# Performance work log

Hardware: AMD Instinct MI355X
Metric: run time of the kernel (lower is better)

The kernel has to match this reference:

```python
import jax, jax.numpy as jnp
import numpy as np

N = 1_000_000  # total_voxels
V = 128        # volume_size


def setup_inputs() -> dict:
    key = jax.random.key(0)
    ks = jax.random.split(key, 10)
    inds = jax.random.randint(ks[0], (N, 3), 0, V, dtype=jnp.int32)
    reference_values = jax.random.normal(ks[1], (1, N), dtype=jnp.float32)
    # SIREN-ish init scales: ~1/sqrt(fan_in) keeps sin() inputs O(1); tiny final
    # layer scale keeps delta_coords sub-voxel (as training would).
    W0 = jax.random.normal(ks[2], (3 * N, 8), dtype=jnp.float32) / np.float32(np.sqrt(3 * N))
    W1 = jax.random.normal(ks[3], (8, 8), dtype=jnp.float32) / np.float32(np.sqrt(8))
    W2 = jax.random.normal(ks[4], (8, 8), dtype=jnp.float32) / np.float32(np.sqrt(8))
    W3 = jax.random.normal(ks[5], (8, 8), dtype=jnp.float32) / np.float32(np.sqrt(8))
    W4 = jax.random.normal(ks[6], (8, 8), dtype=jnp.float32) / np.float32(np.sqrt(8))
    W5 = jax.random.normal(ks[7], (8, 4 * N), dtype=jnp.float32) * np.float32(0.01 / np.sqrt(8))
    z8 = jnp.zeros((8,), jnp.float32)
    return {
        "inds": inds, "reference_values": reference_values,
        "W0": W0, "b0": z8, "W1": W1, "b1": z8, "W2": W2, "b2": z8,
        "W3": W3, "b3": z8, "W4": W4, "b4": z8,
        "W5": W5, "b5": jnp.zeros((4 * N,), jnp.float32),
        "volume_size": V,
    }


def reference(inds, reference_values, W0, b0, W1, b1, W2, b2, W3, b3, W4, b4,
              W5, b5, volume_size):
    n = inds.shape[0]
    factor = 0.5 * volume_size
    # normalized coords buffer: stack (z,y,x) columns -> (1, N, 3) in [-1, 1)
    coords_n = (jnp.stack([inds[:, 2], inds[:, 1], inds[:, 0]], axis=1)[None]
                .astype(jnp.float32) - factor) / factor
    # tiny SIREN MLP on the flattened coord vector (1, 3N)
    x = jnp.sin(coords_n.reshape(1, -1) @ W0 + b0)
    for W, b in ((W1, b1), (W2, b2), (W3, b3), (W4, b4)):
        x = x + jnp.sin(x @ W + b)
    x = (x @ W5 + b5).reshape(1, n, 4)          # (1, N, 4)
    delta_coords, delta_values = x[..., :3], x[..., 3]
    values = jax.nn.relu(reference_values + delta_values)      # (1, N)
    coords = factor * (coords_n + delta_coords) + factor       # voxel-space, (1, N, 3)
    # trilinear 8-corner splat
    bposf = jnp.floor(coords)
    bposi = bposf.astype(jnp.int32)                             # (1, N, 3)
    f = coords - bposf
    fx, fy, fz = f[..., 0], f[..., 1], f[..., 2]
    gx, gy, gz = 1.0 - fx, 1.0 - fy, 1.0 - fz
    bamp = jnp.concatenate([
        values * gx * gy * gz, values * fx * gy * gz,
        values * gx * fy * gz, values * gx * gy * fz,
        values * gx * fy * fz, values * fx * gy * fz,
        values * fx * fy * gz, values * fx * fy * fz,
    ], axis=1)                                                  # (1, 8N)
    offs = jnp.array([[0, 0, 0], [1, 0, 0], [0, 1, 0], [0, 0, 1],
                      [0, 1, 1], [1, 0, 1], [1, 1, 0], [1, 1, 1]], jnp.int32)
    bpos = jnp.concatenate([bposi + o for o in offs], axis=1)   # (1, 8N, 3)
    vol0 = jnp.zeros((values.shape[0], volume_size, volume_size, volume_size),
                     jnp.float32)

    def scatter(vol, p, a):  # out-of-bounds corners are dropped (jax default)
        return vol.at[p[:, 2], p[:, 1], p[:, 0]].add(a)

    return jax.vmap(scatter, in_axes=(0, 0, 0))(vol0, bpos, bamp)
```

## Files before the change

kernel.cpp:

```cpp
#include <hip/hip_runtime.h>
#include <hip/hip_bf16.h>

constexpr int V = 128;
constexpr int NTILES = 512;
constexpr int TD = 17;
constexpr int TSIZE = TD * TD * TD;
constexpr int TPAD = 5120;
constexpr int NS = 16;
constexpr int CAPS = 256;
constexpr int CNT_INTS = NS * NTILES * 16;

__global__ __launch_bounds__(256) void k_reduce_w0(
    const int* __restrict__ inds, const float* __restrict__ W0,
    float* __restrict__ partials, float4* __restrict__ vol4,
    int4* __restrict__ cnt4, int threeN) {
  int g = blockIdx.x * 256 + threadIdx.x;
  vol4[g] = make_float4(0.f, 0.f, 0.f, 0.f);
  if (cnt4 && g < CNT_INTS / 4) cnt4[g] = make_int4(0, 0, 0, 0);

  float acc[8];
#pragma unroll
  for (int k = 0; k < 8; ++k) acc[k] = 0.f;

  int stride = gridDim.x * blockDim.x;
  for (int j = g; j < threeN; j += stride) {
    int c = j % 3;
    float cval = ((float)inds[j + 2 - 2 * c] - 64.0f) * 0.015625f;
    const float4* w = (const float4*)(W0 + (size_t)j * 8);
    float4 a = w[0];
    float4 b = w[1];
    acc[0] += cval * a.x; acc[1] += cval * a.y;
    acc[2] += cval * a.z; acc[3] += cval * a.w;
    acc[4] += cval * b.x; acc[5] += cval * b.y;
    acc[6] += cval * b.z; acc[7] += cval * b.w;
  }

#pragma unroll
  for (int off = 32; off > 0; off >>= 1) {
#pragma unroll
    for (int k = 0; k < 8; ++k) acc[k] += __shfl_down(acc[k], off);
  }

  __shared__ float red[4][8];
  int wave = threadIdx.x >> 6;
  int lane = threadIdx.x & 63;
  if (lane == 0) {
#pragma unroll
    for (int k = 0; k < 8; ++k) red[wave][k] = acc[k];
  }
  __syncthreads();
  if (threadIdx.x < 8) {
    int k = threadIdx.x;
    partials[(size_t)blockIdx.x * 8 + k] = red[0][k] + red[1][k] + red[2][k] + red[3][k];
  }
}

__global__ __launch_bounds__(256) void k_mlp(
    const float* __restrict__ partials, int nb,
    const float* __restrict__ b0,
    const float* __restrict__ W1, const float* __restrict__ b1,
    const float* __restrict__ W2, const float* __restrict__ b2,
    const float* __restrict__ W3, const float* __restrict__ b3,
    const float* __restrict__ W4, const float* __restrict__ b4,
    float* __restrict__ x8_out) {
  __shared__ float red[256];
  __shared__ float accv[8];
  int tid = threadIdx.x;
  int k = tid & 7;
  float s = 0.f;
  for (int b = tid >> 3; b < nb; b += 32) s += partials[(size_t)b * 8 + k];
  red[tid] = s;
  __syncthreads();
  if (tid < 8) {
    float t = 0.f;
    for (int j = tid; j < 256; j += 8) t += red[j];
    accv[tid] = t;
  }
  __syncthreads();
  if (tid == 0) {
    float x[8];
#pragma unroll
    for (int kk = 0; kk < 8; ++kk) x[kk] = sinf(accv[kk] + b0[kk]);
    const float* Ws[4] = {W1, W2, W3, W4};
    const float* bs[4] = {b1, b2, b3, b4};
    for (int l = 0; l < 4; ++l) {
      float t[8];
#pragma unroll
      for (int kk = 0; kk < 8; ++kk) {
        float ss = bs[l][kk];
#pragma unroll
        for (int j = 0; j < 8; ++j) ss += x[j] * Ws[l][j * 8 + kk];
        t[kk] = ss;
      }
#pragma unroll
      for (int kk = 0; kk < 8; ++kk) x[kk] += sinf(t[kk]);
    }
#pragma unroll
    for (int kk = 0; kk < 8; ++kk) x8_out[kk] = x[kk];
  }
}

__device__ inline int tile_of(float cx, float cy, float cz) {
  int bx = (int)floorf(cx), by = (int)floorf(cy), bz = (int)floorf(cz);
  int tx = min(max(bx, 0), V - 1) >> 4;
  int ty = min(max(by, 0), V - 1) >> 4;
  int tz = min(max(bz, 0), V - 1) >> 4;
  return (tz << 6) | (ty << 3) | tx;
}

__device__ inline void scatter_direct(float* vol, float cx, float cy, float cz,
                                      float value) {
  float bxf = floorf(cx), byf = floorf(cy), bzf = floorf(cz);
  int bx = (int)bxf, by = (int)byf, bz = (int)bzf;
  float fx = cx - bxf, fy = cy - byf, fz = cz - bzf;
  float gx = 1.f - fx, gy = 1.f - fy, gz = 1.f - fz;
#pragma unroll
  for (int dz = 0; dz < 2; ++dz)
#pragma unroll
    for (int dy = 0; dy < 2; ++dy)
#pragma unroll
      for (int dx = 0; dx < 2; ++dx) {
        float w = value * (dx ? fx : gx) * (dy ? fy : gy) * (dz ? fz : gz);
        int px = bx + dx, py = by + dy, pz = bz + dz;
        if (px < 0) px += V;
        if (py < 0) py += V;
        if (pz < 0) pz += V;
        if ((unsigned)px < (unsigned)V && (unsigned)py < (unsigned)V &&
            (unsigned)pz < (unsigned)V)
          atomicAdd(vol + ((size_t)pz * V * V + (size_t)py * V + px), w);
      }
}

__global__ __launch_bounds__(256) void k_decode_scatter(
    const int* __restrict__ inds, const float* __restrict__ refv,
    const float* __restrict__ W5, const float* __restrict__ b5,
    const float* __restrict__ x8_buf, float4* __restrict__ srt,
    int* __restrict__ cnt, float* __restrict__ vol, int N) {
  __shared__ float x8[8];
  if (threadIdx.x < 8) x8[threadIdx.x] = x8_buf[threadIdx.x];
  __syncthreads();

  int i = blockIdx.x * 256 + threadIdx.x;
  if (i >= N) return;

  const size_t fourN = (size_t)4 * N;
  float4 o = *(const float4*)(b5 + (size_t)4 * i);
  float out0 = o.x, out1 = o.y, out2 = o.z, out3 = o.w;
#pragma unroll
  for (int k = 0; k < 8; ++k) {
    float xv = x8[k];
    float4 w = *(const float4*)(W5 + (size_t)k * fourN + (size_t)4 * i);
    out0 += xv * w.x; out1 += xv * w.y; out2 += xv * w.z; out3 += xv * w.w;
  }
  float value = refv[i] + out3;
  value = value > 0.f ? value : 0.f;
  if (value <= 0.f) return;

  int i0 = inds[3 * i], i1 = inds[3 * i + 1], i2 = inds[3 * i + 2];
  float cx = (((float)i2 - 64.0f) * 0.015625f + out0) * 64.0f + 64.0f;
  float cy = (((float)i1 - 64.0f) * 0.015625f + out1) * 64.0f + 64.0f;
  float cz = (((float)i0 - 64.0f) * 0.015625f + out2) * 64.0f + 64.0f;

  int t = tile_of(cx, cy, cz);
  int s = blockIdx.x & (NS - 1);
  int slot = s * NTILES + t;
  int pos = atomicAdd(&cnt[slot * 16], 1);
  if (pos < CAPS) {
    srt[(size_t)slot * CAPS + pos] = make_float4(cx, cy, cz, value);
  } else {
    scatter_direct(vol, cx, cy, cz, value);
  }
}

__global__ __launch_bounds__(256) void k_tile(
    const float4* __restrict__ srt, const int* __restrict__ cnt,
    float* __restrict__ priv, float* __restrict__ vol) {
  __shared__ float tl[TSIZE];
  int t = blockIdx.x;
  int ox = (t & 7) << 4, oy = ((t >> 3) & 7) << 4, oz = (t >> 6) << 4;
  for (int j = threadIdx.x; j < TSIZE; j += 256) tl[j] = 0.f;
  __syncthreads();

  for (int s = 0; s < NS; ++s) {
    int slot = s * NTILES + t;
    int c = min(cnt[slot * 16], CAPS);
    const float4* base = srt + (size_t)slot * CAPS;
    for (int i = threadIdx.x; i < c; i += 256) {
      float4 r = base[i];
      float bxf = floorf(r.x), byf = floorf(r.y), bzf = floorf(r.z);
      int bx = (int)bxf, by = (int)byf, bz = (int)bzf;
      float fx = r.x - bxf, fy = r.y - byf, fz = r.z - bzf;
      float gx = 1.f - fx, gy = 1.f - fy, gz = 1.f - fz;
      float value = r.w;

#pragma unroll
      for (int dz = 0; dz < 2; ++dz) {
#pragma unroll
        for (int dy = 0; dy < 2; ++dy) {
#pragma unroll
          for (int dx = 0; dx < 2; ++dx) {
            float w = value * (dx ? fx : gx) * (dy ? fy : gy) * (dz ? fz : gz);
            int px = bx + dx, py = by + dy, pz = bz + dz;
            if (px < 0) px += V;
            if (py < 0) py += V;
            if (pz < 0) pz += V;
            if (px >= V || py >= V || pz >= V) continue;
            int lx = px - ox, ly = py - oy, lz = pz - oz;
            if ((unsigned)lx < (unsigned)TD && (unsigned)ly < (unsigned)TD &&
                (unsigned)lz < (unsigned)TD) {
              atomicAdd(&tl[lz * (TD * TD) + ly * TD + lx], w);
            } else {
              atomicAdd(vol + ((size_t)pz * V * V + (size_t)py * V + px), w);
            }
          }
        }
      }
    }
  }
  __syncthreads();
  for (int j = threadIdx.x; j < TSIZE; j += 256) priv[(size_t)t * TPAD + j] = tl[j];
}

__global__ __launch_bounds__(256) void k_gather(const float* __restrict__ priv,
                                                float* __restrict__ vol) {
  int idx = blockIdx.x * 256 + threadIdx.x;
  int x = idx & 127, y = (idx >> 7) & 127, z = idx >> 14;
  float s = vol[idx];
  int txs[2] = {x >> 4, (x >> 4) - 1}, lxs[2] = {x & 15, 16};
  int tys[2] = {y >> 4, (y >> 4) - 1}, lys[2] = {y & 15, 16};
  int tzs[2] = {z >> 4, (z >> 4) - 1}, lzs[2] = {z & 15, 16};
  int nx = ((x & 15) == 0 && x > 0) ? 2 : 1;
  int ny = ((y & 15) == 0 && y > 0) ? 2 : 1;
  int nz = ((z & 15) == 0 && z > 0) ? 2 : 1;
  for (int iz = 0; iz < nz; ++iz)
    for (int iy = 0; iy < ny; ++iy)
      for (int ix = 0; ix < nx; ++ix) {
        int t = (tzs[iz] << 6) | (tys[iy] << 3) | txs[ix];
        s += priv[(size_t)t * TPAD + lzs[iz] * (TD * TD) + lys[iy] * TD + lxs[ix]];
      }
  vol[idx] = s;
}

__global__ __launch_bounds__(256) void k_scatter(
    const int* __restrict__ inds, const float* __restrict__ refv,
    const float* __restrict__ W5, const float* __restrict__ b5,
    const float* __restrict__ x8_buf, float* __restrict__ vol, int N) {
  __shared__ float x8[8];
  if (threadIdx.x < 8) x8[threadIdx.x] = x8_buf[threadIdx.x];
  __syncthreads();
  int i = blockIdx.x * blockDim.x + threadIdx.x;
  if (i >= N) return;
  const size_t fourN = (size_t)4 * N;
  float4 o = *(const float4*)(b5 + (size_t)4 * i);
  float out0 = o.x, out1 = o.y, out2 = o.z, out3 = o.w;
#pragma unroll
  for (int k = 0; k < 8; ++k) {
    float xv = x8[k];
    float4 w = *(const float4*)(W5 + (size_t)k * fourN + (size_t)4 * i);
    out0 += xv * w.x; out1 += xv * w.y; out2 += xv * w.z; out3 += xv * w.w;
  }
  float value = refv[i] + out3;
  value = value > 0.f ? value : 0.f;
  int i0 = inds[3 * i], i1 = inds[3 * i + 1], i2 = inds[3 * i + 2];
  float cx = (((float)i2 - 64.0f) * 0.015625f + out0) * 64.0f + 64.0f;
  float cy = (((float)i1 - 64.0f) * 0.015625f + out1) * 64.0f + 64.0f;
  float cz = (((float)i0 - 64.0f) * 0.015625f + out2) * 64.0f + 64.0f;
  scatter_direct(vol, cx, cy, cz, value);
}

extern "C" void kernel_launch(void* const* d_in, const int* in_sizes, int n_in,
                              void* d_out, int out_size, void* d_ws, size_t ws_size,
                              hipStream_t stream) {
  const int*   inds = (const int*)d_in[0];
  const float* refv = (const float*)d_in[1];
  const float* W0   = (const float*)d_in[2];
  const float* b0   = (const float*)d_in[3];
  const float* W1   = (const float*)d_in[4];
  const float* b1   = (const float*)d_in[5];
  const float* W2   = (const float*)d_in[6];
  const float* b2   = (const float*)d_in[7];
  const float* W3   = (const float*)d_in[8];
  const float* b3   = (const float*)d_in[9];
  const float* W4   = (const float*)d_in[10];
  const float* b4   = (const float*)d_in[11];
  const float* W5   = (const float*)d_in[12];
  const float* b5   = (const float*)d_in[13];

  int N = in_sizes[0] / 3;
  float* vol = (float*)d_out;
  char* w = (char*)d_ws;

  const int NB_R = 2048;
  float*  x8       = (float*)(w + 0);
  float*  partials = (float*)(w + 256);
  int*    cnt      = (int*)(w + 131072);
  float4* srt      = (float4*)(w + 1048576);
  float*  priv     = (float*)(srt + (size_t)NS * NTILES * CAPS);

  size_t needed = (size_t)1048576 + (size_t)NS * NTILES * CAPS * 16 +
                  (size_t)NTILES * TPAD * 4;

  if (ws_size >= needed) {
    k_reduce_w0<<<NB_R, 256, 0, stream>>>(inds, W0, partials, (float4*)vol,
                                          (int4*)cnt, 3 * N);
    k_mlp<<<1, 256, 0, stream>>>(partials, NB_R, b0, W1, b1, W2, b2, W3, b3, W4, b4, x8);
    k_decode_scatter<<<(N + 255) / 256, 256, 0, stream>>>(inds, refv, W5, b5, x8,
                                                          srt, cnt, vol, N);
    k_tile<<<NTILES, 256, 0, stream>>>(srt, cnt, priv, vol);
    k_gather<<<(V * V * V) / 256, 256, 0, stream>>>(priv, vol);
  } else {
    hipMemsetAsync(d_out, 0, (size_t)out_size * sizeof(float), stream);
    k_reduce_w0<<<NB_R, 256, 0, stream>>>(inds, W0, partials, (float4*)vol,
                                          (int4*)nullptr, 3 * N);
    k_mlp<<<1, 256, 0, stream>>>(partials, NB_R, b0, W1, b1, W2, b2, W3, b3, W4, b4, x8);
    k_scatter<<<(N + 255) / 256, 256, 0, stream>>>(inds, refv, W5, b5, x8, vol, N);
  }
}
```

Measured before the change: 362.3 us.

## Fuse MLP into decode-scatter kernel and use nontemporal loads/stores for streams

After: 382.2 us. 1.05x slower.

```diff
diff --git a/kernel.cpp b/kernel.cpp
--- a/kernel.cpp
+++ b/kernel.cpp
@@ -10,6 +10,17 @@
 constexpr int CAPS = 256;
 constexpr int CNT_INTS = NS * NTILES * 16;
 
+typedef float f4nt __attribute__((ext_vector_type(4)));
+
+__device__ inline float4 ntload4(const float* p) {
+  f4nt v = __builtin_nontemporal_load((const f4nt*)p);
+  return make_float4(v.x, v.y, v.z, v.w);
+}
+__device__ inline void ntstore4(float* p, float4 v) {
+  f4nt t = {v.x, v.y, v.z, v.w};
+  __builtin_nontemporal_store(t, (f4nt*)p);
+}
+
 __global__ __launch_bounds__(256) void k_reduce_w0(
     const int* __restrict__ inds, const float* __restrict__ W0,
     float* __restrict__ partials, float4* __restrict__ vol4,
@@ -26,9 +37,9 @@
   for (int j = g; j < threeN; j += stride) {
     int c = j % 3;
     float cval = ((float)inds[j + 2 - 2 * c] - 64.0f) * 0.015625f;
-    const float4* w = (const float4*)(W0 + (size_t)j * 8);
-    float4 a = w[0];
-    float4 b = w[1];
+    const float* w = W0 + (size_t)j * 8;
+    float4 a = ntload4(w);
+    float4 b = ntload4(w + 4);
     acc[0] += cval * a.x; acc[1] += cval * a.y;
     acc[2] += cval * a.z; acc[3] += cval * a.w;
     acc[4] += cval * b.x; acc[5] += cval * b.y;
@@ -134,22 +145,63 @@
 __global__ __launch_bounds__(256) void k_decode_scatter(
     const int* __restrict__ inds, const float* __restrict__ refv,
     const float* __restrict__ W5, const float* __restrict__ b5,
-    const float* __restrict__ x8_buf, float4* __restrict__ srt,
-    int* __restrict__ cnt, float* __restrict__ vol, int N) {
+    const float* __restrict__ partials, int nb,
+    const float* __restrict__ b0,
+    const float* __restrict__ W1, const float* __restrict__ b1,
+    const float* __restrict__ W2, const float* __restrict__ b2,
+    const float* __restrict__ W3, const float* __restrict__ b3,
+    const float* __restrict__ W4, const float* __restrict__ b4,
+    float4* __restrict__ srt, int* __restrict__ cnt, float* __restrict__ vol,
+    int N) {
+  __shared__ float red[256];
   __shared__ float x8[8];
-  if (threadIdx.x < 8) x8[threadIdx.x] = x8_buf[threadIdx.x];
-  __syncthreads();
+  {
+    int tid = threadIdx.x;
+    int k = tid & 7;
+    float s = 0.f;
+    for (int b = tid >> 3; b < nb; b += 32) s += partials[(size_t)b * 8 + k];
+    red[tid] = s;
+    __syncthreads();
+    if (tid < 8) {
+      float t = 0.f;
+      for (int j = tid; j < 256; j += 8) t += red[j];
+      red[tid] = t;
+    }
+    __syncthreads();
+    if (tid == 0) {
+      float x[8];
+#pragma unroll
+      for (int kk = 0; kk < 8; ++kk) x[kk] = sinf(red[kk] + b0[kk]);
+      const float* Ws[4] = {W1, W2, W3, W4};
+      const float* bs[4] = {b1, b2, b3, b4};
+      for (int l = 0; l < 4; ++l) {
+        float t[8];
+#pragma unroll
+        for (int kk = 0; kk < 8; ++kk) {
+          float ss = bs[l][kk];
+#pragma unroll
+          for (int j = 0; j < 8; ++j) ss += x[j] * Ws[l][j * 8 + kk];
+          t[kk] = ss;
+        }
+#pragma unroll
+        for (int kk = 0; kk < 8; ++kk) x[kk] += sinf(t[kk]);
+      }
+#pragma unroll
+      for (int kk = 0; kk < 8; ++kk) x8[kk] = x[kk];
+    }
+    __syncthreads();
+  }
 
   int i = blockIdx.x * 256 + threadIdx.x;
   if (i >= N) return;
 
   const size_t fourN = (size_t)4 * N;
-  float4 o = *(const float4*)(b5 + (size_t)4 * i);
+  float4 o = ntload4(b5 + (size_t)4 * i);
   float out0 = o.x, out1 = o.y, out2 = o.z, out3 = o.w;
 #pragma unroll
   for (int k = 0; k < 8; ++k) {
     float xv = x8[k];
-    float4 w = *(const float4*)(W5 + (size_t)k * fourN + (size_t)4 * i);
+    float4 w = ntload4(W5 + (size_t)k * fourN + (size_t)4 * i);
     out0 += xv * w.x; out1 += xv * w.y; out2 += xv * w.z; out3 += xv * w.w;
   }
   float value = refv[i] + out3;
@@ -166,7 +218,8 @@
   int slot = s * NTILES + t;
   int pos = atomicAdd(&cnt[slot * 16], 1);
   if (pos < CAPS) {
-    srt[(size_t)slot * CAPS + pos] = make_float4(cx, cy, cz, value);
+    ntstore4((float*)(srt + (size_t)slot * CAPS + pos),
+             make_float4(cx, cy, cz, value));
   } else {
     scatter_direct(vol, cx, cy, cz, value);
   }
@@ -186,7 +239,7 @@
     int c = min(cnt[slot * 16], CAPS);
     const float4* base = srt + (size_t)slot * CAPS;
     for (int i = threadIdx.x; i < c; i += 256) {
-      float4 r = base[i];
+      float4 r = ntload4((const float*)(base + i));
       float bxf = floorf(r.x), byf = floorf(r.y), bzf = floorf(r.z);
       int bx = (int)bxf, by = (int)byf, bz = (int)bzf;
       float fx = r.x - bxf, fy = r.y - byf, fz = r.z - bzf;
@@ -303,9 +356,9 @@
   if (ws_size >= needed) {
     k_reduce_w0<<<NB_R, 256, 0, stream>>>(inds, W0, partials, (float4*)vol,
                                           (int4*)cnt, 3 * N);
-    k_mlp<<<1, 256, 0, stream>>>(partials, NB_R, b0, W1, b1, W2, b2, W3, b3, W4, b4, x8);
-    k_decode_scatter<<<(N + 255) / 256, 256, 0, stream>>>(inds, refv, W5, b5, x8,
-                                                          srt, cnt, vol, N);
+    k_decode_scatter<<<(N + 255) / 256, 256, 0, stream>>>(
+        inds, refv, W5, b5, partials, NB_R, b0, W1, b1, W2, b2, W3, b3, W4, b4,
+        srt, cnt, vol, N);
     k_tile<<<NTILES, 256, 0, stream>>>(srt, cnt, priv, vol);
     k_gather<<<(V * V * V) / 256, 256, 0, stream>>>(priv, vol);
   } else {
```
